# Performance work log

Measured on AMD Instinct MI355X. Metric: run time of the kernel, lower is better.

## Reference

```python
import jax, jax.numpy as jnp
import numpy as np

ZERO = 1e-8
L = 2            # num_gnn_layers
D = 256          # dim_node_features
B = 32           # graphs per batch
NPG = 256        # nodes per graph
N = B * NPG      # total nodes
E = 131072       # edges per edge-type
MAX_TOKENS = 256 # MAX_TOKENS_OF_A_POST
UPD = 0.5        # args.updated_weights_for_A


def _make_edges(k):
    k1, k2, k3 = jax.random.split(k, 3)
    g = jax.random.randint(k1, (E,), 0, B) * NPG          # keep edges within a graph
    src = g + jax.random.randint(k2, (E,), 0, NPG)
    dst = g + jax.random.randint(k3, (E,), 0, NPG)
    return jnp.stack([src, dst]).astype(jnp.int64)


def setup_inputs() -> dict:
    key = jax.random.key(0)
    ks = jax.random.split(key, 12)
    x = jax.random.normal(ks[0], (N, D), dtype=jnp.float32)
    ei_e = _make_edges(ks[1]); ew_e = jax.random.uniform(ks[2], (E,), dtype=jnp.float32)
    ei_p = _make_edges(ks[3]); ew_p = jax.random.uniform(ks[4], (E,), dtype=jnp.float32)
    ei_o = _make_edges(ks[5]); ew_o = jax.random.uniform(ks[6], (E,), dtype=jnp.float32)
    entity_mask = jax.random.randint(ks[7], (B, NPG), 0, 2).astype(bool)
    pattern_mask = jax.random.randint(ks[8], (B, NPG), 0, 2).astype(bool)
    s = 1.0 / np.sqrt(D)
    W_gcn = (jax.random.normal(ks[9], (L, 3, D, D), dtype=jnp.float32) * s)
    b_gcn = jnp.zeros((L, 3, D), dtype=jnp.float32)
    T_dyn = (jax.random.normal(ks[10], (L, D, D), dtype=jnp.float32) * s)
    return {
        'x': x,
        'edge_index_entity': ei_e, 'edge_weight_entity': ew_e,
        'edge_index_pattern': ei_p, 'edge_weight_pattern': ew_p,
        'edge_index_others': ei_o, 'edge_weight_others': ew_o,
        'entity_mask': entity_mask, 'pattern_mask': pattern_mask,
        'W_gcn': W_gcn, 'b_gcn': b_gcn, 'T_dyn': T_dyn,
    }


def _normalized_correlation_matrix(H):
    # cosine-similarity correlation matrix, symmetrically degree-normalized
    nrm = jnp.sqrt(jnp.sum(H * H, axis=1))
    A = (H @ H.T) / (nrm[:, None] * nrm[None, :] + ZERO)
    dinv = 1.0 / jnp.sqrt(jnp.abs(jnp.sum(A, axis=1)) + ZERO)
    return dinv[:, None] * A * dinv[None, :]


def _gcn(H, W, b, ei, ew):
    # GCNConv(add_self_loops=False, normalize=False): scatter-sum of weighted source messages
    msg = (H @ W)[ei[0]] * ew[:, None]                     # [E, D]
    return jax.ops.segment_sum(msg, ei[1], num_segments=N) + b


def _forward(x, we0, wp0, wo0, W_gcn, b_gcn, T_dyn,
             ei_e, ei_p, ei_o, entity_mask, pattern_mask):
    H = x
    A = _normalized_correlation_matrix(H)                  # [N, N]
    for i in range(L):
        if i == 0:
            we, wp, wo = we0, wp0, wo0
        else:
            # diag(one_hot(src) @ A @ one_hot(dst).T) == A[src, dst]
            we = A[ei_e[0], ei_e[1]]
            wp = A[ei_p[0], ei_p[1]]
            wo = A[ei_o[0], ei_o[1]]
        He = _gcn(H, W_gcn[i, 0], b_gcn[i, 0], ei_e, we)
        Hp = _gcn(H, W_gcn[i, 1], b_gcn[i, 1], ei_p, wp)
        Ho = _gcn(H, W_gcn[i, 2], b_gcn[i, 2], ei_o, wo)
        H = jax.nn.relu(He + Hp + Ho)
        A_hat = jax.nn.sigmoid((H @ T_dyn[i]) @ H.T)
        A = (1.0 - UPD) * A + UPD * A_hat
    # per-graph diagonal blocks of A  -> [B, NPG, NPG]
    A4 = A.reshape(B, NPG, B, NPG)
    idx = jnp.arange(B)
    blocks = A4[idx, :, idx, :]
    A_sum = jnp.sum(blocks, axis=-1)                       # [B, NPG]
    ent_cols = jnp.einsum('bij,bj->bi', blocks, entity_mask.astype(A.dtype))
    pat_cols = jnp.einsum('bij,bj->bi', blocks, pattern_mask.astype(A.dtype))
    map_pattern = A_sum - ent_cols
    map_entity = A_sum - pat_cols

    def finish(m):
        mn = jnp.min(m, axis=1, keepdims=True)
        mx = jnp.max(m, axis=1, keepdims=True)
        m = (m - mn) / (mx - mn + ZERO)
        m = m / (jnp.sum(m, axis=1, keepdims=True) + ZERO)
        return m[:, :MAX_TOKENS]                           # padding() with NPG==MAX_TOKENS

    return finish(map_entity), finish(map_pattern)


def reference(x, edge_index_entity, edge_weight_entity,
              edge_index_pattern, edge_weight_pattern,
              edge_index_others, edge_weight_others,
              entity_mask, pattern_mask, W_gcn, b_gcn, T_dyn):
    return _forward(x, edge_weight_entity, edge_weight_pattern, edge_weight_others,
                    W_gcn, b_gcn, T_dyn,
                    edge_index_entity, edge_index_pattern, edge_index_others,
                    entity_mask, pattern_mask)
```

## Files before the change

kernel.cpp:

```cpp
#include <hip/hip_runtime.h>

#define NND   8192
#define DDIM  256
#define NGRP  32
#define ZEROF 1e-8f
#define TSTR  72
#define CCAP 192
#define SM_HALF 49152
#define SM_FULL 49152

typedef unsigned short u16;
typedef __attribute__((ext_vector_type(8))) short short8v;
typedef __attribute__((ext_vector_type(4))) float float4v;

__device__ __forceinline__ void gl16(const u16* g, u16* l) {
  __builtin_amdgcn_global_load_lds(
      (const __attribute__((address_space(1))) unsigned int*)g,
      (__attribute__((address_space(3))) unsigned int*)l, 16, 0, 0);
}

template<int N>
__device__ __forceinline__ void waitv() {
  if constexpr (N == 0)      asm volatile("s_waitcnt vmcnt(0)" ::: "memory");
  else if constexpr (N == 4) asm volatile("s_waitcnt vmcnt(4)" ::: "memory");
  else                       asm volatile("s_waitcnt vmcnt(6)" ::: "memory");
}

__device__ inline u16 f2bf(float x) {
  unsigned u = __float_as_uint(x);
  u += 0x7fffu + ((u >> 16) & 1u);
  return (u16)(u >> 16);
}
__device__ inline float bf2f(u16 h) { return __uint_as_float((unsigned)h << 16); }
__device__ inline void split2(float x, u16& h, u16& l) {
  h = f2bf(x);
  l = f2bf(x - bf2f(h));
}

__device__ inline float wave_sum(float v) {
#pragma unroll
  for (int off = 32; off > 0; off >>= 1) v += __shfl_down(v, off, 64);
  return v;
}

template<int MODE, bool HALF>
__device__ __forceinline__ void mfma_body(
    u16* lds,
    const u16* __restrict__ Ah_g, const u16* __restrict__ Al_g,
    const u16* __restrict__ Bh_g, const u16* __restrict__ Bl_g,
    float* __restrict__ Cf, u16* __restrict__ Ch, u16* __restrict__ Cl,
    const float* __restrict__ nrm, const float* __restrict__ dinv,
    const float* __restrict__ bias,
    int bxm, int bym, int g) {
  const int BS    = HALF ? 8192 : 12288;
  const int NBUF  = HALF ? 3 : 2;
  const int BOFF  = 4096;
  const int BLOFF = 4096 + (HALF ? 2048 : 4096);
  const int NJ = HALF ? 2 : 4;
  const int NLD = HALF ? 4 : 6;
  const int tid = threadIdx.x;
  const int col0 = bxm * (HALF ? 64 : 128);
  const int w = tid >> 6, lane = tid & 63;
  const int lm = lane & 15, lq = lane >> 4;
  const int wr = (w >> 1) * 32, wc = (w & 1) * (HALF ? 32 : 64);
  const int TOTAL = (MODE == 1) ? 24 : 8;

  const int m_ = tid >> 2;
  const int sw = ((tid & 3) ^ (m_ & 3)) * 8;
  const int wbase = (tid >> 6) * 512;

  float4v acc[2][4];
#pragma unroll
  for (int i = 0; i < 2; ++i)
#pragma unroll
    for (int j = 0; j < NJ; ++j) acc[i][j] = (float4v)0.f;

  auto STAGE = [&](int buf, int tt, int kk) {
    u16* base = lds + buf * BS;
    size_t aoff;
    if (MODE == 1)
      aoff = (size_t)(tt * 256 + bym * 64 + m_) * 8192 + (size_t)(g * 256 + kk + sw);
    else if (MODE == 2 || MODE == 3 || MODE == 5)
      aoff = (size_t)(g * 256 + bym * 64 + m_) * 256 + kk + sw;
    else
      aoff = (size_t)(bym * 64 + m_) * 256 + kk + sw;
    gl16(&Ah_g[aoff], base + wbase);
    gl16(&Al_g[aoff], base + 2048 + wbase);
    size_t bbase = (MODE == 1) ? ((size_t)(g * 3 + tt) << 16)
                 : ((MODE == 2 || MODE == 3 || MODE == 5) ? ((size_t)g << 16) : (size_t)0);
    size_t boff = bbase + (size_t)(col0 + m_) * 256 + kk + sw;
    gl16(&Bh_g[boff], base + BOFF + wbase);
    gl16(&Bl_g[boff], base + BLOFF + wbase);
    if (!HALF) {
      size_t boff2 = boff + (size_t)64 * 256;
      gl16(&Bh_g[boff2], base + BOFF + 2048 + wbase);
      gl16(&Bl_g[boff2], base + BLOFF + 2048 + wbase);
    }
  };

  STAGE(0, 0, 0);
  waitv<0>();
  __builtin_amdgcn_s_barrier();
  __builtin_amdgcn_sched_barrier(0);
  int cur = 0;
  for (int step = 0; step < TOTAL; ++step) {
    int nxt = step + 1;
    if (nxt < TOTAL) {
      int tt = (MODE == 1) ? (nxt >> 3) : 0;
      int kk = (MODE == 1) ? ((nxt & 7) * 32) : (nxt * 32);
      int nb = HALF ? (nxt % 3) : (cur ^ 1);
      STAGE(nb, tt, kk);
      waitv<NLD>();
    } else {
      waitv<0>();
    }
    __builtin_amdgcn_s_barrier();
    __builtin_amdgcn_sched_barrier(0);
    u16* base = lds + cur * BS;
    short8v ah[2], al[2], bh[4], bl[4];
#pragma unroll
    for (int i = 0; i < 2; ++i) {
      int r = wr + i * 16 + lm;
      int sa = (lq ^ (r & 3)) * 8;
      ah[i] = *(const short8v*)&base[r * 32 + sa];
      al[i] = *(const short8v*)&base[2048 + r * 32 + sa];
    }
#pragma unroll
    for (int j = 0; j < NJ; ++j) {
      int rb = wc + j * 16 + lm;
      int sb = (lq ^ (rb & 3)) * 8;
      bh[j] = *(const short8v*)&base[BOFF + rb * 32 + sb];
      bl[j] = *(const short8v*)&base[BLOFF + rb * 32 + sb];
    }
    __builtin_amdgcn_s_setprio(1);
#pragma unroll
    for (int i = 0; i < 2; ++i)
#pragma unroll
      for (int j = 0; j < NJ; ++j) {
        acc[i][j] = __builtin_amdgcn_mfma_f32_16x16x32_bf16(ah[i], bh[j], acc[i][j], 0, 0, 0);
        acc[i][j] = __builtin_amdgcn_mfma_f32_16x16x32_bf16(ah[i], bl[j], acc[i][j], 0, 0, 0);
        acc[i][j] = __builtin_amdgcn_mfma_f32_16x16x32_bf16(al[i], bh[j], acc[i][j], 0, 0, 0);
      }
    __builtin_amdgcn_s_setprio(0);
    if (!HALF) {
      __builtin_amdgcn_s_barrier();
    }
    cur = HALF ? (nxt % 3) : (cur ^ 1);
  }

  u16* Tt = lds;
  if (MODE == 2 || MODE == 3 || MODE == 5) {
#pragma unroll
    for (int i = 0; i < 2; ++i) {
#pragma unroll
      for (int r = 0; r < 4; ++r) {
        int grow = g * 256 + bym * 64 + wr + i * 16 + lq * 4 + r;
        float di = 0.f, ni = 0.f;
        if (MODE == 5) { di = dinv[grow]; ni = nrm[grow]; }
#pragma unroll
        for (int j = 0; j < NJ; ++j) {
          int gcol = col0 + wc + j * 16 + lm;
          size_t ci = (size_t)grow * 256 + gcol;
          float v = acc[i][j][r];
          if (MODE == 2) {
            Cf[ci] = v;
          } else if (MODE == 3) {
            Cf[ci] = 0.5f * Cf[ci] + 0.5f * (1.f / (1.f + expf(-v)));
          } else {
            int gj = g * 256 + gcol;
            float scale = di * dinv[gj] / (ni * nrm[gj] + ZEROF);
            Cf[ci] = 0.5f * Cf[ci] * scale + 0.5f * (1.f / (1.f + expf(-v)));
          }
        }
      }
    }
  } else {
    float bsum[8];
    if (MODE == 1) {
#pragma unroll
      for (int i = 0; i < 2; ++i)
#pragma unroll
        for (int r = 0; r < 4; ++r) {
          int d = bym * 64 + wr + i * 16 + lq * 4 + r;
          bsum[i * 4 + r] = bias[d] + bias[256 + d] + bias[512 + d];
        }
    }
    u16 hv[32], lv[32];
#pragma unroll
    for (int i = 0; i < 2; ++i)
#pragma unroll
      for (int j = 0; j < NJ; ++j)
#pragma unroll
        for (int r = 0; r < 4; ++r) {
          float v = acc[i][j][r];
          if (MODE == 1) v = fmaxf(v + bsum[i * 4 + r], 0.f);
          split2(v, hv[(i * 4 + r) * NJ + j], lv[(i * 4 + r) * NJ + j]);
        }
    int ebase1 = (MODE == 1) ? (g * 256 + col0) : col0;
    int ebase2 = bym * 64;
    size_t estride = (MODE == 0) ? 8192 : 256;
#pragma unroll
    for (int ph = 0; ph < 2; ++ph) {
      __syncthreads();
      const u16* sv = ph ? lv : hv;
#pragma unroll
      for (int i = 0; i < 2; ++i)
#pragma unroll
        for (int j = 0; j < NJ; ++j)
#pragma unroll
          for (int r = 0; r < 4; ++r)
            Tt[(wc + j * 16 + lm) * TSTR + wr + i * 16 + lq * 4 + r] = sv[(i * 4 + r) * NJ + j];
      __syncthreads();
      u16* dst = ph ? Cl : Ch;
      int cc0 = tid >> 3, mm0 = (tid & 7) * 8;
#pragma unroll
      for (int it = 0; it < (HALF ? 2 : 4); ++it) {
        int cc = it * 32 + cc0;
        short8v v = *(const short8v*)&Tt[cc * TSTR + mm0];
        *(short8v*)&dst[(size_t)(ebase1 + cc) * estride + ebase2 + mm0] = v;
      }
    }
  }
}

__device__ __forceinline__ void mbuild_body(
    float* tile, int bid, int l,
    const uint2* __restrict__ recs2, const int* __restrict__ bcnt2,
    const float* __restrict__ Abuf, u16* __restrict__ Mbh, u16* __restrict__ Mbl) {
  const int tid = threadIdx.x;
  int gt = bid >> 3, chunk = bid & 7;
  int g = gt / 3;
  float4 z = make_float4(0.f, 0.f, 0.f, 0.f);
#pragma unroll
  for (int k = 0; k < 8; ++k) ((float4*)tile)[k * 256 + tid] = z;
  __syncthreads();
#pragma unroll
  for (int c = 0; c < 8; ++c) {
    int cnt = bcnt2[bid * 8 + c];
    const uint2* rp = &recs2[(size_t)bid * (8 * CCAP) + (size_t)c * CCAP];
    for (int k = tid; k < cnt; k += 256) {
      uint2 r = rp[k];
      int s = r.x & 255, d5 = (r.x >> 8) & 31;
      float w = l ? Abuf[(size_t)(g * 256 + s) * 256 + chunk * 32 + d5]
                  : __uint_as_float(r.y);
      atomicAdd(&tile[d5 * 256 + s], w);
    }
  }
  __syncthreads();
  size_t base4 = ((size_t)gt << 14) + ((size_t)chunk << 11);
#pragma unroll
  for (int k = 0; k < 8; ++k) {
    float4 f = ((float4*)tile)[k * 256 + tid];
    ushort4 h, lo;
    split2(f.x, h.x, lo.x); split2(f.y, h.y, lo.y);
    split2(f.z, h.z, lo.z); split2(f.w, h.w, lo.w);
    ((ushort4*)Mbh)[base4 + k * 256 + tid] = h;
    ((ushort4*)Mbl)[base4 + k * 256 + tid] = lo;
  }
}

__global__ void k_prep(const int* __restrict__ e0, const int* __restrict__ e1,
                       const int* __restrict__ e2, const unsigned char* __restrict__ m0,
                       const unsigned char* __restrict__ m1,
                       const float* __restrict__ W, const float* __restrict__ T,
                       const float* __restrict__ x,
                       const float* __restrict__ ew0, const float* __restrict__ ew1,
                       const float* __restrict__ ew2,
                       float* __restrict__ emf, float* __restrict__ pmf,
                       u16* __restrict__ Wth, u16* __restrict__ Wtl,
                       u16* __restrict__ sct, uint2* __restrict__ recs,
                       float* __restrict__ nrm, float* __restrict__ Spart,
                       u16* __restrict__ Hh, u16* __restrict__ Hl,
                       int E_, int nCvt, int nBkt) {
  __shared__ float tile[32][33];
  __shared__ float inv[64];
  __shared__ int nz[1];
  __shared__ unsigned int hcnt[768];
  __shared__ unsigned int hoff[768];
  __shared__ unsigned int ppart[256];
  __shared__ uint2 stage[768];
  const int b = blockIdx.x, tid = threadIdx.x;
  if (b < nCvt) {
    if (tid == 0) nz[0] = 0;
    __syncthreads();
    int i4 = tid * 4;
    int c = (m0[i4 + 1] != 0) + (m0[i4 + 2] != 0) + (m0[i4 + 3] != 0);
    if (c) atomicAdd(&nz[0], c);
    __syncthreads();
    int fM = (nz[0] == 0);
    int i = b * 256 + tid;
    if (i < NND) {
      unsigned char v = fM ? m0[4 * i] : m0[i];
      emf[i] = 1.f - (float)(v != 0);
    } else {
      int j = i - NND;
      unsigned char v = fM ? m1[4 * j] : m1[j];
      pmf[j] = 1.f - (float)(v != 0);
    }
  } else if (b < nCvt + nBkt) {
    if (tid == 0) nz[0] = 0;
    hcnt[tid] = 0; hcnt[tid + 256] = 0; hcnt[tid + 512] = 0;
    __syncthreads();
    if (e0[2 * tid + 1] != 0) atomicAdd(&nz[0], 1);
    __syncthreads();
    int fE = (nz[0] == 0);
    int e = (b - nCvt) * 256 + tid;
    bool valid = (e < E_);
    int mybid[3]; unsigned int myrec[3]; float myw[3];
    if (valid) {
#pragma unroll
      for (int t = 0; t < 3; ++t) {
        const int* ei = (t == 0) ? e0 : ((t == 1) ? e1 : e2);
        int src = fE ? ei[2 * e] : ei[e];
        int dst = fE ? ei[2 * (E_ + e)] : ei[E_ + e];
        int g = src >> 8, s = src & 255, d = dst & 255;
        mybid[t] = ((g * 3 + t) << 3) | (d >> 5);
        myrec[t] = (unsigned)(((d & 31) << 8) | s);
        myw[t] = (t == 0 ? ew0 : (t == 1 ? ew1 : ew2))[e];
        atomicAdd(&hcnt[mybid[t]], 1u);
      }
    }
    __syncthreads();
    unsigned c0 = hcnt[3 * tid], c1 = hcnt[3 * tid + 1], c2 = hcnt[3 * tid + 2];
    unsigned tsum = c0 + c1 + c2;
    ppart[tid] = tsum;
    __syncthreads();
    for (int off = 1; off < 256; off <<= 1) {
      unsigned v = (tid >= off) ? ppart[tid - off] : 0u;
      __syncthreads();
      ppart[tid] += v;
      __syncthreads();
    }
    unsigned base = ppart[tid] - tsum;
    hoff[3 * tid] = base;
    hoff[3 * tid + 1] = base + c0;
    hoff[3 * tid + 2] = base + c0 + c1;
    __syncthreads();
#pragma unroll
    for (int k = 0; k < 3; ++k) {
      int bin = tid + k * 256;
      unsigned cc = hcnt[bin]; if (cc > 31u) cc = 31u;
      sct[(size_t)(b - nCvt) * 768 + bin] = (u16)(hoff[bin] | (cc << 11));
    }
    __syncthreads();
    if (valid) {
#pragma unroll
      for (int t = 0; t < 3; ++t) {
        unsigned slot = atomicAdd(&hoff[mybid[t]], 1u);
        stage[slot] = make_uint2(myrec[t], __float_as_uint(myw[t]));
      }
    }
    __syncthreads();
    uint2* dstp = &recs[(size_t)(b - nCvt) * 768];
    dstp[tid] = stage[tid];
    dstp[tid + 256] = stage[tid + 256];
    dstp[tid + 512] = stage[tid + 512];
  } else if (b < nCvt + nBkt + 512) {
    int bb = b - nCvt - nBkt;
    int mat = bb >> 6, rem = bb & 63;
    int k0 = (rem >> 3) * 32, n0 = (rem & 7) * 32;
    const float* src = (mat < 6) ? (W + (size_t)mat * 65536) : (T + (size_t)(mat - 6) * 65536);
    int r = tid >> 3, c4 = (tid & 7) * 4;
    const float4 v = *(const float4*)&src[(size_t)(k0 + r) * 256 + n0 + c4];
    tile[r][c4 + 0] = v.x; tile[r][c4 + 1] = v.y; tile[r][c4 + 2] = v.z; tile[r][c4 + 3] = v.w;
    __syncthreads();
    float o[4] = {tile[c4 + 0][r], tile[c4 + 1][r], tile[c4 + 2][r], tile[c4 + 3][r]};
    u16 hh[4], ll[4];
#pragma unroll
    for (int q = 0; q < 4; ++q) split2(o[q], hh[q], ll[q]);
    size_t off = (size_t)mat * 65536 + (size_t)(n0 + r) * 256 + k0 + c4;
    *(ushort4*)&Wth[off] = *(ushort4*)hh;
    *(ushort4*)&Wtl[off] = *(ushort4*)ll;
  } else {
    int bn = b - nCvt - nBkt - 512;
    int n0 = bn * 64;
    int w = tid >> 6, lane = tid & 63;
    for (int it = 0; it < 16; ++it) {
      int nl = it * 4 + w;
      int node = n0 + nl;
      const float4 v = *(const float4*)&x[(size_t)node * 256 + lane * 4];
      u16 hh[4], ll[4];
      split2(v.x, hh[0], ll[0]); split2(v.y, hh[1], ll[1]);
      split2(v.z, hh[2], ll[2]); split2(v.w, hh[3], ll[3]);
      *(ushort4*)&Hh[(size_t)node * 256 + lane * 4] = *(ushort4*)hh;
      *(ushort4*)&Hl[(size_t)node * 256 + lane * 4] = *(ushort4*)ll;
      float s = wave_sum(v.x * v.x + v.y * v.y + v.z * v.z + v.w * v.w);
      if (lane == 0) { float nr = sqrtf(s); nrm[node] = nr; inv[nl] = 1.f / nr; }
    }
    __syncthreads();
    float s = 0.f;
    for (int i = 0; i < 64; ++i) s += x[(size_t)(n0 + i) * 256 + tid] * inv[i];
    Spart[bn * 256 + tid] = s;
  }
}

__global__ void k_reorder(const u16* __restrict__ sct, const uint2* __restrict__ recs,
                          uint2* __restrict__ recs2, int* __restrict__ bcnt2, int nBkt) {
  const int wid = blockIdx.x * 4 + (threadIdx.x >> 6);
  const int lane = threadIdx.x & 63;
  const int bid = wid >> 3;
  const int c = wid & 7;
  const int nseg = nBkt >> 3;
  unsigned cnt = 0, start = 0;
  int bb = c * nseg + lane;
  if (lane < nseg) {
    unsigned sc = sct[(size_t)bb * 768 + bid];
    start = sc & 2047u; cnt = sc >> 11;
  }
  unsigned pre = cnt;
#pragma unroll
  for (int off = 1; off < 64; off <<= 1) {
    unsigned v = __shfl_up(pre, off, 64);
    if (lane >= off) pre += v;
  }
  unsigned excl = pre - cnt;
  unsigned total = __shfl(pre, 63, 64);
  uint2* dst = &recs2[(size_t)bid * (8 * CCAP) + (size_t)c * CCAP];
  const uint2* rp = &recs[(size_t)bb * 768 + start];
  for (unsigned k = 0; k < cnt; ++k) {
    unsigned o = excl + k;
    if (o < CCAP) dst[o] = rp[k];
  }
  if (lane == 0) bcnt2[bid * 8 + c] = (total > CCAP) ? CCAP : total;
}

__global__ __launch_bounds__(256, 2) void k_stageA(
    const u16* __restrict__ Hinh, const u16* __restrict__ Hinl,
    const u16* __restrict__ Wth, const u16* __restrict__ Wtl,
    u16* __restrict__ XWTh, u16* __restrict__ XWTl,
    const uint2* __restrict__ recs2, const int* __restrict__ bcnt2,
    u16* __restrict__ Mbh, u16* __restrict__ Mbl,
    float* __restrict__ Abuf,
    const float* __restrict__ x, const float* __restrict__ Spart,
    const float* __restrict__ nrm, float* __restrict__ dinv) {
  extern __shared__ u16 lds[];
  const int b = blockIdx.x;
  if (b < 768) {
    mfma_body<0, false>(lds, Hinh, Hinl, Wth, Wtl,
                        nullptr, XWTh, XWTl, nullptr, nullptr, nullptr,
                        b >> 7, b & 127, 0);
  } else if (b < 1536) {
    mbuild_body((float*)lds, b - 768, 0, recs2, bcnt2, nullptr, Mbh, Mbl);
  } else if (b < 2048) {
    int bb = b - 1536;
    int g = bb & 31, r = bb >> 5;
    mfma_body<2, true>(lds, Hinh, Hinl, Hinh, Hinl, Abuf, nullptr, nullptr,
                       nullptr, nullptr, nullptr, r >> 2, r & 3, g);
  } else {
    float* Sl = (float*)lds;
    const int tid = threadIdx.x;
    float s = 0.f;
    for (int bb = 0; bb < 128; ++bb) s += Spart[bb * 256 + tid];
    Sl[tid] = s;
    __syncthreads();
    int base = (b - 2048) * 64;
    int w = tid >> 6, lane = tid & 63;
    const float4 sv = *(const float4*)&Sl[lane * 4];
    for (int it = 0; it < 16; ++it) {
      int node = base + it * 4 + w;
      const float4 v = *(const float4*)&x[(size_t)node * 256 + lane * 4];
      float s2 = wave_sum(v.x * sv.x + v.y * sv.y + v.z * sv.z + v.w * sv.w);
      if (lane == 0) {
        float rowsum = s2 / nrm[node];
        dinv[node] = rsqrtf(fabsf(rowsum) + ZEROF);
      }
    }
  }
}

__global__ __launch_bounds__(256, 2) void k_stageA2(
    const u16* __restrict__ H2h, const u16* __restrict__ H2l,
    const u16* __restrict__ Wth, const u16* __restrict__ Wtl,
    u16* __restrict__ XWTh, u16* __restrict__ XWTl,
    const uint2* __restrict__ recs2, const int* __restrict__ bcnt2,
    const float* __restrict__ Abuf,
    u16* __restrict__ Mbh, u16* __restrict__ Mbl) {
  extern __shared__ u16 lds[];
  const int b = blockIdx.x;
  if (b < 768) {
    mfma_body<0, false>(lds, H2h, H2l, Wth + (size_t)768 * 256, Wtl + (size_t)768 * 256,
                        nullptr, XWTh, XWTl, nullptr, nullptr, nullptr,
                        b >> 7, b & 127, 0);
  } else {
    mbuild_body((float*)lds, b - 768, 1, recs2, bcnt2, Abuf, Mbh, Mbl);
  }
}

__global__ __launch_bounds__(256, 2) void k_stageB(
    const u16* __restrict__ XWTh, const u16* __restrict__ XWTl,
    const u16* __restrict__ Mbh, const u16* __restrict__ Mbl,
    u16* __restrict__ Houth, u16* __restrict__ Houtl, const float* __restrict__ bias) {
  extern __shared__ u16 lds[];
  const int b = blockIdx.x;
  int g = b & 31, r = b >> 5;
  mfma_body<1, true>(lds, XWTh, XWTl, Mbh, Mbl,
                     nullptr, Houth, Houtl, nullptr, nullptr, bias,
                     r >> 2, r & 3, g);
}

__global__ __launch_bounds__(256, 2) void k_stageC(
    const u16* __restrict__ Wth, const u16* __restrict__ Wtl, int l,
    const u16* __restrict__ Hh, const u16* __restrict__ Hl,
    u16* __restrict__ tmph, u16* __restrict__ tmpl) {
  extern __shared__ u16 lds[];
  const int b = blockIdx.x;
  mfma_body<4, true>(lds, Wth + (size_t)(6 + l) * 65536, Wtl + (size_t)(6 + l) * 65536,
                     Hh, Hl, nullptr, tmph, tmpl, nullptr, nullptr, nullptr,
                     b & 127, b >> 7, 0);
}

__global__ __launch_bounds__(256, 2) void k_stageD(
    const u16* __restrict__ tmph, const u16* __restrict__ tmpl,
    const u16* __restrict__ Hh, const u16* __restrict__ Hl,
    float* __restrict__ Abuf,
    const float* __restrict__ nrm, const float* __restrict__ dinv, int scaled) {
  extern __shared__ u16 lds[];
  const int b = blockIdx.x;
  int g = b & 31, r = b >> 5;
  if (scaled)
    mfma_body<5, true>(lds, tmph, tmpl, Hh, Hl, Abuf, nullptr, nullptr,
                       nrm, dinv, nullptr, r >> 2, r & 3, g);
  else
    mfma_body<3, true>(lds, tmph, tmpl, Hh, Hl, Abuf, nullptr, nullptr,
                       nullptr, nullptr, nullptr, r >> 2, r & 3, g);
}

__global__ void k_maps(const float* __restrict__ Abuf, const float* __restrict__ emf,
                       const float* __restrict__ pmf, float* __restrict__ out) {
  __shared__ float sme[256], smp[256], red[256];
  const int g = blockIdx.x, tid = threadIdx.x, w = tid >> 6, lane = tid & 63;
  const int j0 = g * 256 + lane * 4;
  const float4 pmv = *(const float4*)&pmf[j0];
  const float4 emv = *(const float4*)&emf[j0];
  for (int it = 0; it < 64; ++it) {
    int nl = it * 4 + w;
    const float4 a = *(const float4*)&Abuf[((size_t)g * 256 + nl) * 256 + lane * 4];
    float me = a.x * pmv.x + a.y * pmv.y + a.z * pmv.z + a.w * pmv.w;
    float mp = a.x * emv.x + a.y * emv.y + a.z * emv.z + a.w * emv.w;
#pragma unroll
    for (int off = 32; off > 0; off >>= 1) {
      me += __shfl_down(me, off, 64);
      mp += __shfl_down(mp, off, 64);
    }
    if (lane == 0) { sme[nl] = me; smp[nl] = mp; }
  }
  __syncthreads();
  for (int which = 0; which < 2; ++which) {
    float v = which ? smp[tid] : sme[tid];
    red[tid] = v; __syncthreads();
    for (int s = 128; s > 0; s >>= 1) { if (tid < s) red[tid] = fminf(red[tid], red[tid + s]); __syncthreads(); }
    float mn = red[0]; __syncthreads();
    red[tid] = v; __syncthreads();
    for (int s = 128; s > 0; s >>= 1) { if (tid < s) red[tid] = fmaxf(red[tid], red[tid + s]); __syncthreads(); }
    float mx = red[0]; __syncthreads();
    float m = (v - mn) / (mx - mn + ZEROF);
    red[tid] = m; __syncthreads();
    for (int s = 128; s > 0; s >>= 1) { if (tid < s) red[tid] += red[tid + s]; __syncthreads(); }
    float sum = red[0]; __syncthreads();
    out[which * NND + g * 256 + tid] = m / (sum + ZEROF);
  }
}

extern "C" void kernel_launch(void* const* d_in, const int* in_sizes, int n_in,
                              void* d_out, int out_size, void* d_ws, size_t ws_size,
                              hipStream_t stream) {
  const float* x = (const float*)d_in[0];
  const unsigned char* em_raw = (const unsigned char*)d_in[7];
  const unsigned char* pm_raw = (const unsigned char*)d_in[8];
  const float* W  = (const float*)d_in[9];
  const float* bg = (const float*)d_in[10];
  const float* T  = (const float*)d_in[11];
  float* out = (float*)d_out;
  const int E_ = in_sizes[2];

  const int nCvt = (2 * NND) / 256;
  const int nBkt = (E_ + 255) / 256;

  float* ws = (float*)d_ws;
  size_t o = 0;
  float* Abuf = ws + o; o += (size_t)NND * 256;
  u16* Mbh_l0 = (u16*)(ws + o); o += (size_t)NGRP * 3 * 65536 / 2;
  u16* Mbl_l0 = (u16*)(ws + o); o += (size_t)NGRP * 3 * 65536 / 2;
  u16* Mbh_l1 = (u16*)(ws + o); o += (size_t)NGRP * 3 * 65536 / 2;
  u16* Mbl_l1 = (u16*)(ws + o); o += (size_t)NGRP * 3 * 65536 / 2;
  u16* Hh   = (u16*)(ws + o); o += (size_t)NND * 256 / 2;
  u16* Hl   = (u16*)(ws + o); o += (size_t)NND * 256 / 2;
  u16* H2h  = (u16*)(ws + o); o += (size_t)NND * 256 / 2;
  u16* H2l  = (u16*)(ws + o); o += (size_t)NND * 256 / 2;
  u16* tmph = (u16*)(ws + o); o += (size_t)NND * 256 / 2;
  u16* tmpl = (u16*)(ws + o); o += (size_t)NND * 256 / 2;
  u16* XWTh = (u16*)(ws + o); o += (size_t)768 * NND / 2;
  u16* XWTl = (u16*)(ws + o); o += (size_t)768 * NND / 2;
  u16* Wth  = (u16*)(ws + o); o += (size_t)8 * 65536 / 2;
  u16* Wtl  = (u16*)(ws + o); o += (size_t)8 * 65536 / 2;
  float* nrm   = ws + o; o += NND;
  float* dinv  = ws + o; o += NND;
  float* Spart = ws + o; o += 128 * 256;
  float* emf   = ws + o; o += NND;
  float* pmf   = ws + o; o += NND;
  u16* sct     = (u16*)(ws + o); o += (size_t)nBkt * 768 / 2;
  uint2* recs  = (uint2*)(ws + o); o += (size_t)nBkt * 768 * 2;
  uint2* recs2 = (uint2*)(ws + o); o += (size_t)768 * 8 * CCAP * 2;
  int* bcnt2   = (int*)(ws + o); o += (size_t)768 * 8;

  const float* ew0 = (const float*)d_in[2];
  const float* ew1 = (const float*)d_in[4];
  const float* ew2 = (const float*)d_in[6];

  k_prep<<<nCvt + nBkt + 512 + 128, 256, 0, stream>>>(
      (const int*)d_in[1], (const int*)d_in[3], (const int*)d_in[5], em_raw, pm_raw,
      W, T, x, ew0, ew1, ew2, emf, pmf, Wth, Wtl, sct, recs,
      nrm, Spart, Hh, Hl, E_, nCvt, nBkt);

  k_reorder<<<1536, 256, 0, stream>>>(sct, recs, recs2, bcnt2, nBkt);

  k_stageA<<<2176, 256, SM_FULL, stream>>>(Hh, Hl, Wth, Wtl, XWTh, XWTl,
                                           recs2, bcnt2, Mbh_l0, Mbl_l0, Abuf,
                                           x, Spart, nrm, dinv);
  k_stageB<<<512, 256, SM_HALF, stream>>>(XWTh, XWTl, Mbh_l0, Mbl_l0, H2h, H2l, bg);
  k_stageC<<<512, 256, SM_HALF, stream>>>(Wth, Wtl, 0, H2h, H2l, tmph, tmpl);
  k_stageD<<<512, 256, SM_HALF, stream>>>(tmph, tmpl, H2h, H2l, Abuf, nrm, dinv, 1);

  k_stageA2<<<1536, 256, SM_FULL, stream>>>(H2h, H2l, Wth, Wtl, XWTh, XWTl,
                                            recs2, bcnt2, Abuf, Mbh_l1, Mbl_l1);
  k_stageB<<<512, 256, SM_HALF, stream>>>(XWTh, XWTl, Mbh_l1, Mbl_l1, Hh, Hl, bg + 768);
  k_stageC<<<512, 256, SM_HALF, stream>>>(Wth, Wtl, 1, Hh, Hl, tmph, tmpl);
  k_stageD<<<512, 256, SM_HALF, stream>>>(tmph, tmpl, Hh, Hl, Abuf, nullptr, nullptr, 0);

  k_maps<<<NGRP, 256, 0, stream>>>(Abuf, emf, pmf, out);
}
```

Before: 252.4 us.

## Bucket edges directly via global atomic counters, dropping the reorder kernel

Edge bucketing no longer builds per-block histograms with prefix scans and a separate reorder kernel. Each edge now claims a slot in a global per-bucket counter with one atomic and writes its record straight into the final capped bucket array. Counters are padded to 64 bytes to reduce contention on shared cache lines and are cleared with a memset each call. This removes one kernel launch and an intermediate buffer round-trip, at the cost of global atomic traffic and record order within a bucket that varies from run to run.

```diff
diff --git a/kernel.cpp b/kernel.cpp
--- a/kernel.cpp
+++ b/kernel.cpp
@@ -53,7 +53,6 @@
     const float* __restrict__ bias,
     int bxm, int bym, int g) {
   const int BS    = HALF ? 8192 : 12288;
-  const int NBUF  = HALF ? 3 : 2;
   const int BOFF  = 4096;
   const int BLOFF = 4096 + (HALF ? 2048 : 4096);
   const int NJ = HALF ? 2 : 4;
@@ -225,7 +224,7 @@
 
 __device__ __forceinline__ void mbuild_body(
     float* tile, int bid, int l,
-    const uint2* __restrict__ recs2, const int* __restrict__ bcnt2,
+    const uint2* __restrict__ recs2, const int* __restrict__ bcntP,
     const float* __restrict__ Abuf, u16* __restrict__ Mbh, u16* __restrict__ Mbl) {
   const int tid = threadIdx.x;
   int gt = bid >> 3, chunk = bid & 7;
@@ -236,8 +235,9 @@
   __syncthreads();
 #pragma unroll
   for (int c = 0; c < 8; ++c) {
-    int cnt = bcnt2[bid * 8 + c];
-    const uint2* rp = &recs2[(size_t)bid * (8 * CCAP) + (size_t)c * CCAP];
+    int cnt = bcntP[(bid * 8 + c) * 16];
+    if (cnt > CCAP) cnt = CCAP;
+    const uint2* rp = &recs2[(size_t)(bid * 8 + c) * CCAP];
     for (int k = tid; k < cnt; k += 256) {
       uint2 r = rp[k];
       int s = r.x & 255, d5 = (r.x >> 8) & 31;
@@ -268,17 +268,13 @@
                        const float* __restrict__ ew2,
                        float* __restrict__ emf, float* __restrict__ pmf,
                        u16* __restrict__ Wth, u16* __restrict__ Wtl,
-                       u16* __restrict__ sct, uint2* __restrict__ recs,
+                       uint2* __restrict__ recs2, int* __restrict__ bcntP,
                        float* __restrict__ nrm, float* __restrict__ Spart,
                        u16* __restrict__ Hh, u16* __restrict__ Hl,
                        int E_, int nCvt, int nBkt) {
   __shared__ float tile[32][33];
   __shared__ float inv[64];
   __shared__ int nz[1];
-  __shared__ unsigned int hcnt[768];
-  __shared__ unsigned int hoff[768];
-  __shared__ unsigned int ppart[256];
-  __shared__ uint2 stage[768];
   const int b = blockIdx.x, tid = threadIdx.x;
   if (b < nCvt) {
     if (tid == 0) nz[0] = 0;
@@ -299,62 +295,27 @@
     }
   } else if (b < nCvt + nBkt) {
     if (tid == 0) nz[0] = 0;
-    hcnt[tid] = 0; hcnt[tid + 256] = 0; hcnt[tid + 512] = 0;
     __syncthreads();
     if (e0[2 * tid + 1] != 0) atomicAdd(&nz[0], 1);
     __syncthreads();
     int fE = (nz[0] == 0);
     int e = (b - nCvt) * 256 + tid;
-    bool valid = (e < E_);
-    int mybid[3]; unsigned int myrec[3]; float myw[3];
-    if (valid) {
+    int ch = (b - nCvt) / (nBkt >> 3);
+    if (e < E_) {
 #pragma unroll
       for (int t = 0; t < 3; ++t) {
         const int* ei = (t == 0) ? e0 : ((t == 1) ? e1 : e2);
         int src = fE ? ei[2 * e] : ei[e];
         int dst = fE ? ei[2 * (E_ + e)] : ei[E_ + e];
         int g = src >> 8, s = src & 255, d = dst & 255;
-        mybid[t] = ((g * 3 + t) << 3) | (d >> 5);
-        myrec[t] = (unsigned)(((d & 31) << 8) | s);
-        myw[t] = (t == 0 ? ew0 : (t == 1 ? ew1 : ew2))[e];
-        atomicAdd(&hcnt[mybid[t]], 1u);
+        int bid = ((g * 3 + t) << 3) | (d >> 5);
+        float wgt = (t == 0 ? ew0 : (t == 1 ? ew1 : ew2))[e];
+        int slot = atomicAdd(&bcntP[(bid * 8 + ch) * 16], 1);
+        if (slot < CCAP)
+          recs2[(size_t)(bid * 8 + ch) * CCAP + slot] =
+              make_uint2((unsigned)(((d & 31) << 8) | s), __float_as_uint(wgt));
       }
     }
-    __syncthreads();
-    unsigned c0 = hcnt[3 * tid], c1 = hcnt[3 * tid + 1], c2 = hcnt[3 * tid + 2];
-    unsigned tsum = c0 + c1 + c2;
-    ppart[tid] = tsum;
-    __syncthreads();
-    for (int off = 1; off < 256; off <<= 1) {
-      unsigned v = (tid >= off) ? ppart[tid - off] : 0u;
-      __syncthreads();
-      ppart[tid] += v;
-      __syncthreads();
-    }
-    unsigned base = ppart[tid] - tsum;
-    hoff[3 * tid] = base;
-    hoff[3 * tid + 1] = base + c0;
-    hoff[3 * tid + 2] = base + c0 + c1;
-    __syncthreads();
-#pragma unroll
-    for (int k = 0; k < 3; ++k) {
-      int bin = tid + k * 256;
-      unsigned cc = hcnt[bin]; if (cc > 31u) cc = 31u;
-      sct[(size_t)(b - nCvt) * 768 + bin] = (u16)(hoff[bin] | (cc << 11));
-    }
-    __syncthreads();
-    if (valid) {
-#pragma unroll
-      for (int t = 0; t < 3; ++t) {
-        unsigned slot = atomicAdd(&hoff[mybid[t]], 1u);
-        stage[slot] = make_uint2(myrec[t], __float_as_uint(myw[t]));
-      }
-    }
-    __syncthreads();
-    uint2* dstp = &recs[(size_t)(b - nCvt) * 768];
-    dstp[tid] = stage[tid];
-    dstp[tid + 256] = stage[tid + 256];
-    dstp[tid + 512] = stage[tid + 512];
   } else if (b < nCvt + nBkt + 512) {
     int bb = b - nCvt - nBkt;
     int mat = bb >> 6, rem = bb & 63;
@@ -394,41 +355,11 @@
   }
 }
 
-__global__ void k_reorder(const u16* __restrict__ sct, const uint2* __restrict__ recs,
-                          uint2* __restrict__ recs2, int* __restrict__ bcnt2, int nBkt) {
-  const int wid = blockIdx.x * 4 + (threadIdx.x >> 6);
-  const int lane = threadIdx.x & 63;
-  const int bid = wid >> 3;
-  const int c = wid & 7;
-  const int nseg = nBkt >> 3;
-  unsigned cnt = 0, start = 0;
-  int bb = c * nseg + lane;
-  if (lane < nseg) {
-    unsigned sc = sct[(size_t)bb * 768 + bid];
-    start = sc & 2047u; cnt = sc >> 11;
-  }
-  unsigned pre = cnt;
-#pragma unroll
-  for (int off = 1; off < 64; off <<= 1) {
-    unsigned v = __shfl_up(pre, off, 64);
-    if (lane >= off) pre += v;
-  }
-  unsigned excl = pre - cnt;
-  unsigned total = __shfl(pre, 63, 64);
-  uint2* dst = &recs2[(size_t)bid * (8 * CCAP) + (size_t)c * CCAP];
-  const uint2* rp = &recs[(size_t)bb * 768 + start];
-  for (unsigned k = 0; k < cnt; ++k) {
-    unsigned o = excl + k;
-    if (o < CCAP) dst[o] = rp[k];
-  }
-  if (lane == 0) bcnt2[bid * 8 + c] = (total > CCAP) ? CCAP : total;
-}
-
 __global__ __launch_bounds__(256, 2) void k_stageA(
     const u16* __restrict__ Hinh, const u16* __restrict__ Hinl,
     const u16* __restrict__ Wth, const u16* __restrict__ Wtl,
     u16* __restrict__ XWTh, u16* __restrict__ XWTl,
-    const uint2* __restrict__ recs2, const int* __restrict__ bcnt2,
+    const uint2* __restrict__ recs2, const int* __restrict__ bcntP,
     u16* __restrict__ Mbh, u16* __restrict__ Mbl,
     float* __restrict__ Abuf,
     const float* __restrict__ x, const float* __restrict__ Spart,
@@ -440,7 +371,7 @@
                         nullptr, XWTh, XWTl, nullptr, nullptr, nullptr,
                         b >> 7, b & 127, 0);
   } else if (b < 1536) {
-    mbuild_body((float*)lds, b - 768, 0, recs2, bcnt2, nullptr, Mbh, Mbl);
+    mbuild_body((float*)lds, b - 768, 0, recs2, bcntP, nullptr, Mbh, Mbl);
   } else if (b < 2048) {
     int bb = b - 1536;
     int g = bb & 31, r = bb >> 5;
@@ -472,7 +403,7 @@
     const u16* __restrict__ H2h, const u16* __restrict__ H2l,
     const u16* __restrict__ Wth, const u16* __restrict__ Wtl,
     u16* __restrict__ XWTh, u16* __restrict__ XWTl,
-    const uint2* __restrict__ recs2, const int* __restrict__ bcnt2,
+    const uint2* __restrict__ recs2, const int* __restrict__ bcntP,
     const float* __restrict__ Abuf,
     u16* __restrict__ Mbh, u16* __restrict__ Mbl) {
   extern __shared__ u16 lds[];
@@ -482,7 +413,7 @@
                         nullptr, XWTh, XWTl, nullptr, nullptr, nullptr,
                         b >> 7, b & 127, 0);
   } else {
-    mbuild_body((float*)lds, b - 768, 1, recs2, bcnt2, Abuf, Mbh, Mbl);
+    mbuild_body((float*)lds, b - 768, 1, recs2, bcntP, Abuf, Mbh, Mbl);
   }
 }
 
@@ -598,31 +529,29 @@
   float* Spart = ws + o; o += 128 * 256;
   float* emf   = ws + o; o += NND;
   float* pmf   = ws + o; o += NND;
-  u16* sct     = (u16*)(ws + o); o += (size_t)nBkt * 768 / 2;
-  uint2* recs  = (uint2*)(ws + o); o += (size_t)nBkt * 768 * 2;
   uint2* recs2 = (uint2*)(ws + o); o += (size_t)768 * 8 * CCAP * 2;
-  int* bcnt2   = (int*)(ws + o); o += (size_t)768 * 8;
+  int* bcntP   = (int*)(ws + o); o += (size_t)768 * 8 * 16;
 
   const float* ew0 = (const float*)d_in[2];
   const float* ew1 = (const float*)d_in[4];
   const float* ew2 = (const float*)d_in[6];
 
+  hipMemsetAsync(bcntP, 0, (size_t)768 * 8 * 16 * sizeof(int), stream);
+
   k_prep<<<nCvt + nBkt + 512 + 128, 256, 0, stream>>>(
       (const int*)d_in[1], (const int*)d_in[3], (const int*)d_in[5], em_raw, pm_raw,
-      W, T, x, ew0, ew1, ew2, emf, pmf, Wth, Wtl, sct, recs,
+      W, T, x, ew0, ew1, ew2, emf, pmf, Wth, Wtl, recs2, bcntP,
       nrm, Spart, Hh, Hl, E_, nCvt, nBkt);
 
-  k_reorder<<<1536, 256, 0, stream>>>(sct, recs, recs2, bcnt2, nBkt);
-
   k_stageA<<<2176, 256, SM_FULL, stream>>>(Hh, Hl, Wth, Wtl, XWTh, XWTl,
-                                           recs2, bcnt2, Mbh_l0, Mbl_l0, Abuf,
+                                           recs2, bcntP, Mbh_l0, Mbl_l0, Abuf,
                                            x, Spart, nrm, dinv);
   k_stageB<<<512, 256, SM_HALF, stream>>>(XWTh, XWTl, Mbh_l0, Mbl_l0, H2h, H2l, bg);
   k_stageC<<<512, 256, SM_HALF, stream>>>(Wth, Wtl, 0, H2h, H2l, tmph, tmpl);
   k_stageD<<<512, 256, SM_HALF, stream>>>(tmph, tmpl, H2h, H2l, Abuf, nrm, dinv, 1);
 
   k_stageA2<<<1536, 256, SM_FULL, stream>>>(H2h, H2l, Wth, Wtl, XWTh, XWTl,
-                                            recs2, bcnt2, Abuf, Mbh_l1, Mbl_l1);
+                                            recs2, bcntP, Abuf, Mbh_l1, Mbl_l1);
   k_stageB<<<512, 256, SM_HALF, stream>>>(XWTh, XWTl, Mbh_l1, Mbl_l1, Hh, Hl, bg + 768);
   k_stageC<<<512, 256, SM_HALF, stream>>>(Wth, Wtl, 1, Hh, Hl, tmph, tmpl);
   k_stageD<<<512, 256, SM_HALF, stream>>>(tmph, tmpl, Hh, Hl, Abuf, nullptr, nullptr, 0);
```

Result: slower. 264.2 us (+4.7%).
